# Performance work log

Measured on AMD Instinct MI355X. Metric: run time of the kernel, lower is better.

Reference implementation:

```python
import jax, jax.numpy as jnp
import numpy as np

N = 4_000_000  # observations
C = 2000       # cameras
B = 1000       # base poses
R = 8          # relative (rig) poses
P = 500_000    # 3D points


def quat_to_rotmat(q):
    # q: [..., 4] in pypose (x, y, z, w) order; normalized before use (as pypose does)
    q = q / jnp.linalg.norm(q, axis=-1, keepdims=True)
    x, y, z, w = q[..., 0], q[..., 1], q[..., 2], q[..., 3]
    r00 = 1 - 2 * (y * y + z * z); r01 = 2 * (x * y - w * z); r02 = 2 * (x * z + w * y)
    r10 = 2 * (x * y + w * z); r11 = 1 - 2 * (x * x + z * z); r12 = 2 * (y * z - w * x)
    r20 = 2 * (x * z - w * y); r21 = 2 * (y * z + w * x); r22 = 1 - 2 * (x * x + y * y)
    return jnp.stack([jnp.stack([r00, r01, r02], -1),
                      jnp.stack([r10, r11, r12], -1),
                      jnp.stack([r20, r21, r22], -1)], -2)


def setup_inputs() -> dict:
    key = jax.random.key(0)
    ks = jax.random.split(key, 10)
    cam = jax.random.randint(ks[0], (N,), 0, C)
    pt = jax.random.randint(ks[1], (N,), 0, P)
    pix = jax.random.normal(ks[2], (N, 2), dtype=jnp.float32) * 100.0 + 500.0
    observations = jnp.concatenate([cam[:, None].astype(jnp.float32),
                                    pt[:, None].astype(jnp.float32), pix], axis=1)
    # base poses: random rotation, translation near z=+10 so points project in front of camera
    tb = jax.random.normal(ks[3], (B, 3), dtype=jnp.float32) * 0.1 + jnp.array([0.0, 0.0, 10.0])
    qb = jax.random.normal(ks[4], (B, 4), dtype=jnp.float32)
    qb = qb / jnp.linalg.norm(qb, axis=-1, keepdims=True)
    base_poses = jnp.concatenate([tb, qb], axis=1)
    # relative poses: small rig offsets, near-identity rotation
    tr = jax.random.normal(ks[5], (R, 3), dtype=jnp.float32) * 0.05
    qr = jnp.concatenate([jax.random.normal(ks[6], (R, 3), dtype=jnp.float32) * 0.01,
                          jnp.ones((R, 1), jnp.float32)], axis=1)
    qr = qr / jnp.linalg.norm(qr, axis=-1, keepdims=True)
    relative_poses = jnp.concatenate([tr, qr], axis=1)
    points = jax.random.normal(ks[7], (P, 3), dtype=jnp.float32)
    # pinhole intrinsics K = [[f,0,cx],[0,f,cy],[0,0,1]]
    f = 1000.0 + jax.random.normal(ks[8], (C,), dtype=jnp.float32) * 10.0
    z = jnp.zeros((C,), jnp.float32); o = jnp.ones((C,), jnp.float32)
    cx = 500.0 * o; cy = 500.0 * o
    intrinsics = jnp.stack([jnp.stack([f, z, cx], -1),
                            jnp.stack([z, f, cy], -1),
                            jnp.stack([z, z, o], -1)], -2)
    base_idx = jax.random.randint(ks[9], (C,), 0, B)
    rel_idx = jax.random.randint(jax.random.fold_in(key, 11), (C,), 0, R)
    has_rel = jax.random.bernoulli(jax.random.fold_in(key, 12), 0.5, (C,))
    rel_idx = jnp.where(has_rel, rel_idx, -1)
    lookup_indices = jnp.stack([base_idx, rel_idx], axis=1).astype(jnp.int32)
    return {"observations": observations, "base_poses": base_poses,
            "relative_poses": relative_poses, "points": points,
            "intrinsics": intrinsics, "lookup_indices": lookup_indices}


def reference(observations, base_poses, relative_poses, points, intrinsics, lookup_indices):
    cam = observations[:, 0].astype(jnp.int32)
    pt = observations[:, 1].astype(jnp.int32)
    pixels_measured = observations[:, 2:]
    bpi = lookup_indices[cam, 0]          # [N]
    rpi = lookup_indices[cam, 1]          # [N], -1 means no relative pose
    mask = rpi != -1
    rel_safe = jnp.where(mask, rpi, 0)
    sel_base = base_poses[bpi]            # [N,7]
    t_base = sel_base[:, :3]
    R_base = quat_to_rotmat(sel_base[:, 3:])  # [N,3,3]
    sel_rel = relative_poses[rel_safe]    # [N,7]
    t_rel = sel_rel[:, :3]
    R_rel = quat_to_rotmat(sel_rel[:, 3:])
    R_comp = jnp.einsum('nij,njk->nik', R_base, R_rel)
    t_comp = t_base + jnp.einsum('nij,nj->ni', R_base, t_rel)
    R_final = jnp.where(mask[:, None, None], R_comp, R_base)
    t_final = jnp.where(mask[:, None], t_comp, t_base)
    p_cam = jnp.einsum('nij,nj->ni', R_final, points[pt]) + t_final
    proj = jnp.einsum('nij,nj->ni', intrinsics[cam], p_cam)
    pred = proj[:, :2] / proj[:, 2:3]
    return (pred - pixels_measured).ravel()
```

## Files before the change

### kernel.cpp

```cpp
#include <hip/hip_runtime.h>
#include <hip/hip_fp16.h>
#include <math.h>

#define C_MAX 2000

typedef float f32x4 __attribute__((ext_vector_type(4)));

__device__ __forceinline__ unsigned pkh(float a, float b) {
    union { unsigned u; __half2 h; } x;
    x.h = __floats2half2_rn(a, b);
    return x.u;
}
__device__ __forceinline__ float2 uph(unsigned u) {
    union { unsigned u; __half2 h; } x;
    x.u = u;
    return make_float2(__low2float(x.h), __high2float(x.h));
}

__device__ __forceinline__ void quat_to_R(float q0, float q1, float q2, float q3, float R[9]) {
    float inv = 1.0f / sqrtf(q0 * q0 + q1 * q1 + q2 * q2 + q3 * q3);
    float x = q0 * inv, y = q1 * inv, z = q2 * inv, w = q3 * inv;
    R[0] = 1.0f - 2.0f * (y * y + z * z);
    R[1] = 2.0f * (x * y - w * z);
    R[2] = 2.0f * (x * z + w * y);
    R[3] = 2.0f * (x * y + w * z);
    R[4] = 1.0f - 2.0f * (x * x + z * z);
    R[5] = 2.0f * (y * z - w * x);
    R[6] = 2.0f * (x * z - w * y);
    R[7] = 2.0f * (y * z + w * x);
    R[8] = 1.0f - 2.0f * (x * x + y * y);
}

__global__ void cam_precompute(const float* __restrict__ base_poses,
                               const float* __restrict__ rel_poses,
                               const float* __restrict__ intr,
                               const int* __restrict__ lookup,
                               uint4* __restrict__ cam_packed,
                               int C) {
    int c = blockIdx.x * blockDim.x + threadIdx.x;
    if (c >= C) return;
    int bpi = lookup[2 * c + 0];
    int rpi = lookup[2 * c + 1];
    bool has_rel = (rpi != -1);
    int rs = has_rel ? rpi : 0;

    const float* bp = base_poses + 7 * bpi;
    float tb0 = bp[0], tb1 = bp[1], tb2 = bp[2];
    float Rb[9];
    quat_to_R(bp[3], bp[4], bp[5], bp[6], Rb);

    const float* rp = rel_poses + 7 * rs;
    float Rr[9];
    quat_to_R(rp[3], rp[4], rp[5], rp[6], Rr);

    float Rf[9], tf0, tf1, tf2;
    if (has_rel) {
        #pragma unroll
        for (int i = 0; i < 3; ++i) {
            #pragma unroll
            for (int j = 0; j < 3; ++j) {
                Rf[3 * i + j] = Rb[3 * i + 0] * Rr[0 + j]
                              + Rb[3 * i + 1] * Rr[3 + j]
                              + Rb[3 * i + 2] * Rr[6 + j];
            }
        }
        tf0 = tb0 + Rb[0] * rp[0] + Rb[1] * rp[1] + Rb[2] * rp[2];
        tf1 = tb1 + Rb[3] * rp[0] + Rb[4] * rp[1] + Rb[5] * rp[2];
        tf2 = tb2 + Rb[6] * rp[0] + Rb[7] * rp[1] + Rb[8] * rp[2];
    } else {
        #pragma unroll
        for (int i = 0; i < 9; ++i) Rf[i] = Rb[i];
        tf0 = tb0; tf1 = tb1; tf2 = tb2;
    }

    const float* K = intr + 9 * c;
    float M[9], v[3];
    #pragma unroll
    for (int i = 0; i < 3; ++i) {
        #pragma unroll
        for (int j = 0; j < 3; ++j) {
            M[3 * i + j] = K[3 * i + 0] * Rf[0 + j]
                         + K[3 * i + 1] * Rf[3 + j]
                         + K[3 * i + 2] * Rf[6 + j];
        }
        v[i] = K[3 * i + 0] * tf0 + K[3 * i + 1] * tf1 + K[3 * i + 2] * tf2;
    }

    uint4 w0, w1;
    w0.x = pkh(M[0], M[1]);
    w0.y = pkh(M[2], M[3]);
    w0.z = pkh(M[4], M[5]);
    w0.w = pkh(M[6], M[7]);
    w1.x = pkh(M[8], 0.0f);
    w1.y = __float_as_uint(v[0]);
    w1.z = __float_as_uint(v[1]);
    w1.w = __float_as_uint(v[2]);
    cam_packed[2 * c + 0] = w0;
    cam_packed[2 * c + 1] = w1;
}

__global__ void pack_points(const float* __restrict__ pts, uint2* __restrict__ ph, int P) {
    int i = blockIdx.x * blockDim.x + threadIdx.x;
    if (i < P) {
        float x = pts[3 * i + 0], y = pts[3 * i + 1], z = pts[3 * i + 2];
        uint2 q;
        q.x = pkh(x, y);
        q.y = pkh(z, 0.0f);
        ph[i] = q;
    }
}

__device__ __forceinline__ float2 project_one(const uint4& A, const uint4& B,
                                              const uint2& q, float mx, float my) {
    float2 m01 = uph(A.x);
    float2 m23 = uph(A.y);
    float2 m45 = uph(A.z);
    float2 m67 = uph(A.w);
    float2 m8_ = uph(B.x);
    float v0 = __uint_as_float(B.y);
    float v1 = __uint_as_float(B.z);
    float v2 = __uint_as_float(B.w);
    float2 xy = uph(q.x);
    float2 zp = uph(q.y);
    float px = xy.x, py = xy.y, pz = zp.x;

    float jx = m01.x * px + m01.y * py + m23.x * pz + v0;
    float jy = m23.y * px + m45.x * py + m45.y * pz + v1;
    float jz = m67.x * px + m67.y * py + m8_.x * pz + v2;
    float iz = 1.0f / jz;
    return make_float2(jx * iz - mx, jy * iz - my);
}

__launch_bounds__(1024, 8)
__global__ void residual_lds(const float4* __restrict__ obs,
                             const uint2* __restrict__ pts,
                             const uint4* __restrict__ camg,
                             float4* __restrict__ out,
                             int G,
                             long N,
                             int C) {
    __shared__ uint4 s_cam[2 * C_MAX];
    int nent = 2 * C;
    for (int i = threadIdx.x; i < nent; i += blockDim.x)
        s_cam[i] = camg[i];
    __syncthreads();

    int stride = gridDim.x * blockDim.x;
    for (int g = blockIdx.x * blockDim.x + threadIdx.x; g < G; g += stride) {
        long base = (long)g * 4;
        if (base + 3 < N) {
            float4 o0 = obs[base + 0];
            float4 o1 = obs[base + 1];
            float4 o2 = obs[base + 2];
            float4 o3 = obs[base + 3];

            int c0 = (int)o0.x, p0 = (int)o0.y;
            int c1 = (int)o1.x, p1 = (int)o1.y;
            int c2 = (int)o2.x, p2 = (int)o2.y;
            int c3 = (int)o3.x, p3 = (int)o3.y;

            uint2 q0 = pts[p0], q1 = pts[p1], q2 = pts[p2], q3 = pts[p3];

            uint4 A0 = s_cam[2 * c0], B0 = s_cam[2 * c0 + 1];
            uint4 A1 = s_cam[2 * c1], B1 = s_cam[2 * c1 + 1];
            uint4 A2 = s_cam[2 * c2], B2 = s_cam[2 * c2 + 1];
            uint4 A3 = s_cam[2 * c3], B3 = s_cam[2 * c3 + 1];

            float2 r0 = project_one(A0, B0, q0, o0.z, o0.w);
            float2 r1 = project_one(A1, B1, q1, o1.z, o1.w);
            float2 r2 = project_one(A2, B2, q2, o2.z, o2.w);
            float2 r3 = project_one(A3, B3, q3, o3.z, o3.w);

            f32x4 r01 = {r0.x, r0.y, r1.x, r1.y};
            f32x4 r23 = {r2.x, r2.y, r3.x, r3.y};
            f32x4* outv = (f32x4*)out;
            __builtin_nontemporal_store(r01, &outv[2 * g + 0]);
            __builtin_nontemporal_store(r23, &outv[2 * g + 1]);
        } else {
            float2* out2 = (float2*)out;
            for (long i = base; i < N; ++i) {
                float4 o = obs[i];
                int cam = (int)o.x;
                int pt = (int)o.y;
                uint4 A = s_cam[2 * cam], B = s_cam[2 * cam + 1];
                uint2 q = pts[pt];
                float2 r = project_one(A, B, q, o.z, o.w);
                out2[i] = r;
            }
        }
    }
}

extern "C" void kernel_launch(void* const* d_in, const int* in_sizes, int n_in,
                              void* d_out, int out_size, void* d_ws, size_t ws_size,
                              hipStream_t stream) {
    const float* obs = (const float*)d_in[0];
    const float* base_poses = (const float*)d_in[1];
    const float* rel_poses = (const float*)d_in[2];
    const float* points = (const float*)d_in[3];
    const float* intr = (const float*)d_in[4];
    const int* lookup = (const int*)d_in[5];

    long N = in_sizes[0] / 4;
    int P = in_sizes[3] / 3;
    int C = in_sizes[5] / 2;

    uint4* cam_packed = (uint4*)d_ws;
    uint2* pts_h = (uint2*)((char*)d_ws + (size_t)C_MAX * 32);

    cam_precompute<<<(C + 255) / 256, 256, 0, stream>>>(
        base_poses, rel_poses, intr, lookup, cam_packed, C);
    pack_points<<<(P + 255) / 256, 256, 0, stream>>>(points, pts_h, P);

    int G = (int)((N + 3) / 4);
    int threads = 1024;
    int blocks = 512;
    residual_lds<<<blocks, threads, 0, stream>>>(
        (const float4*)obs, pts_h, cam_packed, (float4*)d_out, G, N, C);
}
```

Measured before the change: 51.94 us.

## Drop LDS camera staging, read camera table from global with one-shot grid

Removes the per-block copy of the packed camera table into shared memory and its barrier. Camera entries are now read straight from global memory, where the small 64 KB table should stay cache-resident. The persistent grid-stride launch of 1024-thread blocks becomes a one-thread-per-four-observations launch with 256-thread blocks. Observation loads are marked nontemporal to avoid polluting the cache. The trade is scattered global/L2 camera reads in place of LDS reads, in exchange for dropping the 512 redundant table copies.

After: 81.30 us. 1.57x slower.

```diff
diff --git a/kernel.cpp b/kernel.cpp
--- a/kernel.cpp
+++ b/kernel.cpp
@@ -1,8 +1,6 @@
 #include <hip/hip_runtime.h>
 #include <hip/hip_fp16.h>
 #include <math.h>
-
-#define C_MAX 2000
 
 typedef float f32x4 __attribute__((ext_vector_type(4)));
 
@@ -35,7 +33,7 @@
                                const float* __restrict__ rel_poses,
                                const float* __restrict__ intr,
                                const int* __restrict__ lookup,
-                               uint4* __restrict__ cam_packed,
+                               uint4* __restrict__ cam,
                                int C) {
     int c = blockIdx.x * blockDim.x + threadIdx.x;
     if (c >= C) return;
@@ -95,8 +93,8 @@
     w1.y = __float_as_uint(v[0]);
     w1.z = __float_as_uint(v[1]);
     w1.w = __float_as_uint(v[2]);
-    cam_packed[2 * c + 0] = w0;
-    cam_packed[2 * c + 1] = w1;
+    cam[2 * c + 0] = w0;
+    cam[2 * c + 1] = w1;
 }
 
 __global__ void pack_points(const float* __restrict__ pts, uint2* __restrict__ ph, int P) {
@@ -131,62 +129,54 @@
     return make_float2(jx * iz - mx, jy * iz - my);
 }
 
-__launch_bounds__(1024, 8)
-__global__ void residual_lds(const float4* __restrict__ obs,
-                             const uint2* __restrict__ pts,
-                             const uint4* __restrict__ camg,
-                             float4* __restrict__ out,
-                             int G,
-                             long N,
-                             int C) {
-    __shared__ uint4 s_cam[2 * C_MAX];
-    int nent = 2 * C;
-    for (int i = threadIdx.x; i < nent; i += blockDim.x)
-        s_cam[i] = camg[i];
-    __syncthreads();
-
-    int stride = gridDim.x * blockDim.x;
-    for (int g = blockIdx.x * blockDim.x + threadIdx.x; g < G; g += stride) {
-        long base = (long)g * 4;
-        if (base + 3 < N) {
-            float4 o0 = obs[base + 0];
-            float4 o1 = obs[base + 1];
-            float4 o2 = obs[base + 2];
-            float4 o3 = obs[base + 3];
-
-            int c0 = (int)o0.x, p0 = (int)o0.y;
-            int c1 = (int)o1.x, p1 = (int)o1.y;
-            int c2 = (int)o2.x, p2 = (int)o2.y;
-            int c3 = (int)o3.x, p3 = (int)o3.y;
-
-            uint2 q0 = pts[p0], q1 = pts[p1], q2 = pts[p2], q3 = pts[p3];
-
-            uint4 A0 = s_cam[2 * c0], B0 = s_cam[2 * c0 + 1];
-            uint4 A1 = s_cam[2 * c1], B1 = s_cam[2 * c1 + 1];
-            uint4 A2 = s_cam[2 * c2], B2 = s_cam[2 * c2 + 1];
-            uint4 A3 = s_cam[2 * c3], B3 = s_cam[2 * c3 + 1];
-
-            float2 r0 = project_one(A0, B0, q0, o0.z, o0.w);
-            float2 r1 = project_one(A1, B1, q1, o1.z, o1.w);
-            float2 r2 = project_one(A2, B2, q2, o2.z, o2.w);
-            float2 r3 = project_one(A3, B3, q3, o3.z, o3.w);
-
-            f32x4 r01 = {r0.x, r0.y, r1.x, r1.y};
-            f32x4 r23 = {r2.x, r2.y, r3.x, r3.y};
-            f32x4* outv = (f32x4*)out;
-            __builtin_nontemporal_store(r01, &outv[2 * g + 0]);
-            __builtin_nontemporal_store(r23, &outv[2 * g + 1]);
-        } else {
-            float2* out2 = (float2*)out;
-            for (long i = base; i < N; ++i) {
-                float4 o = obs[i];
-                int cam = (int)o.x;
-                int pt = (int)o.y;
-                uint4 A = s_cam[2 * cam], B = s_cam[2 * cam + 1];
-                uint2 q = pts[pt];
-                float2 r = project_one(A, B, q, o.z, o.w);
-                out2[i] = r;
-            }
+__launch_bounds__(256, 8)
+__global__ void residual_g(const f32x4* __restrict__ obsv,
+                           const uint2* __restrict__ pts,
+                           const uint4* __restrict__ cam,
+                           float4* __restrict__ out,
+                           int G,
+                           long N) {
+    int g = blockIdx.x * blockDim.x + threadIdx.x;
+    if (g >= G) return;
+    long base = (long)g * 4;
+    if (base + 3 < N) {
+        f32x4 o0 = __builtin_nontemporal_load(&obsv[base + 0]);
+        f32x4 o1 = __builtin_nontemporal_load(&obsv[base + 1]);
+        f32x4 o2 = __builtin_nontemporal_load(&obsv[base + 2]);
+        f32x4 o3 = __builtin_nontemporal_load(&obsv[base + 3]);
+
+        int c0 = (int)o0.x, p0 = (int)o0.y;
+        int c1 = (int)o1.x, p1 = (int)o1.y;
+        int c2 = (int)o2.x, p2 = (int)o2.y;
+        int c3 = (int)o3.x, p3 = (int)o3.y;
+
+        uint2 q0 = pts[p0], q1 = pts[p1], q2 = pts[p2], q3 = pts[p3];
+
+        uint4 A0 = cam[2 * c0], B0 = cam[2 * c0 + 1];
+        uint4 A1 = cam[2 * c1], B1 = cam[2 * c1 + 1];
+        uint4 A2 = cam[2 * c2], B2 = cam[2 * c2 + 1];
+        uint4 A3 = cam[2 * c3], B3 = cam[2 * c3 + 1];
+
+        float2 r0 = project_one(A0, B0, q0, o0.z, o0.w);
+        float2 r1 = project_one(A1, B1, q1, o1.z, o1.w);
+        float2 r2 = project_one(A2, B2, q2, o2.z, o2.w);
+        float2 r3 = project_one(A3, B3, q3, o3.z, o3.w);
+
+        f32x4 r01 = {r0.x, r0.y, r1.x, r1.y};
+        f32x4 r23 = {r2.x, r2.y, r3.x, r3.y};
+        f32x4* outv = (f32x4*)out;
+        __builtin_nontemporal_store(r01, &outv[2 * g + 0]);
+        __builtin_nontemporal_store(r23, &outv[2 * g + 1]);
+    } else {
+        float2* out2 = (float2*)out;
+        for (long i = base; i < N; ++i) {
+            f32x4 o = obsv[i];
+            int c = (int)o.x;
+            int pt = (int)o.y;
+            uint4 A = cam[2 * c], B = cam[2 * c + 1];
+            uint2 q = pts[pt];
+            float2 r = project_one(A, B, q, o.z, o.w);
+            out2[i] = r;
         }
     }
 }
@@ -205,16 +195,16 @@
     int P = in_sizes[3] / 3;
     int C = in_sizes[5] / 2;
 
-    uint4* cam_packed = (uint4*)d_ws;
-    uint2* pts_h = (uint2*)((char*)d_ws + (size_t)C_MAX * 32);
+    uint4* cam = (uint4*)d_ws;
+    uint2* pts_h = (uint2*)((char*)d_ws + (size_t)2048 * 32);
 
     cam_precompute<<<(C + 255) / 256, 256, 0, stream>>>(
-        base_poses, rel_poses, intr, lookup, cam_packed, C);
+        base_poses, rel_poses, intr, lookup, cam, C);
     pack_points<<<(P + 255) / 256, 256, 0, stream>>>(points, pts_h, P);
 
     int G = (int)((N + 3) / 4);
-    int threads = 1024;
-    int blocks = 512;
-    residual_lds<<<blocks, threads, 0, stream>>>(
-        (const float4*)obs, pts_h, cam_packed, (float4*)d_out, G, N, C);
-}
+    int threads = 256;
+    int blocks = (G + threads - 1) / threads;
+    residual_g<<<blocks, threads, 0, stream>>>(
+        (const f32x4*)obs, pts_h, cam, (float4*)d_out, G, N);
+}
```
